# Performance work log

Measured on AMD Instinct MI355X. Metric: run time of the kernel, lower is better.

Reference implementation:

```python
import jax, jax.numpy as jnp
import numpy as np

N_NODES = 50000
N_EDGES = 800000
N_FEATS = 128
E_FEATS = 64
N_OUT = 64
E_OUT = 32
HID = 128  # num_hids = [128]; f lifts node features to this dim
N_STEPS = 3


def _mlp(v, W1, b1, W2, b2):
    # one hidden ReLU layer, linear output (same structure for all 7 transforms)
    return jax.nn.relu(v @ W1 + b1) @ W2 + b2


def _init_mlp(key, d_in, d_hid, d_out, scale=0.05):
    k1, k2 = jax.random.split(key)
    return (jax.random.normal(k1, (d_in, d_hid), jnp.float32) * scale,
            jnp.zeros((d_hid,), jnp.float32),
            jax.random.normal(k2, (d_hid, d_out), jnp.float32) * scale,
            jnp.zeros((d_out,), jnp.float32))


def setup_inputs() -> dict:
    key = jax.random.key(0)
    ks = jax.random.split(key, 10)
    x = jax.random.normal(ks[0], (N_NODES, N_FEATS), jnp.float32)
    xe = jax.random.normal(ks[1], (N_EDGES, E_FEATS), jnp.float32)
    edge_index = jax.random.randint(ks[2], (2, N_EDGES), 0, N_NODES, jnp.int32)
    inp = {"x": x, "xe": xe, "edge_index": edge_index}
    names = ["f", "g", "h", "k1", "k2", "k", "l"]
    dims = {"f": (N_FEATS, HID), "g": (HID, HID), "h": (HID, N_OUT),
            "k1": (HID, HID), "k2": (HID, HID), "k": (E_FEATS, HID), "l": (HID, E_OUT)}
    for i, nm in enumerate(names):
        d_in, d_out = dims[nm]
        W1, b1, W2, b2 = _init_mlp(ks[3 + i], d_in, HID, d_out)
        inp[nm + "_W1"], inp[nm + "_b1"] = W1, b1
        inp[nm + "_W2"], inp[nm + "_b2"] = W2, b2
    return inp


def reference(x, xe, edge_index,
              f_W1, f_b1, f_W2, f_b2,
              g_W1, g_b1, g_W2, g_b2,
              h_W1, h_b1, h_W2, h_b2,
              k1_W1, k1_b1, k1_W2, k1_b2,
              k2_W1, k2_b1, k2_W2, k2_b2,
              k_W1, k_b1, k_W2, k_b2,
              l_W1, l_b1, l_W2, l_b2):
    src, dst = edge_index[0], edge_index[1]
    # 1. y = f(x): lift node features to HID
    y = _mlp(x, f_W1, f_b1, f_W2, f_b2)
    # 2. message passing: y <- g(sum over neighbors of y) + y
    for _ in range(N_STEPS):
        agg = jax.ops.segment_sum(y[src], dst, num_segments=N_NODES)  # [N, HID]
        y = _mlp(agg, g_W1, g_b1, g_W2, g_b2) + y
    # 3. node output z = h(y)
    node_out = _mlp(y, h_W1, h_b1, h_W2, h_b2)  # [N, N_OUT]
    # 4. edge output z_ij = l(k1(y_i) + k2(y_j) + k(x_ij))
    e_hid = (_mlp(y[src], k1_W1, k1_b1, k1_W2, k1_b2)
             + _mlp(y[dst], k2_W1, k2_b1, k2_W2, k2_b2)
             + _mlp(xe, k_W1, k_b1, k_W2, k_b2))  # [E, HID]
    edge_out = _mlp(e_hid, l_W1, l_b1, l_W2, l_b2)  # [E, E_OUT]
    return node_out, edge_out
```

## Files before the change

### kernel.cpp

```cpp
#include <hip/hip_runtime.h>
#include <hip/hip_bf16.h>

namespace {

constexpr int NN = 50000;
constexpr int NE = 800000;

typedef __attribute__((ext_vector_type(8))) short bf16x8;
typedef __attribute__((ext_vector_type(4))) float f32x4;

__device__ __forceinline__ short f2bf(float f) {
  union { __hip_bfloat16 h; short s; } u;
  u.h = __float2bfloat16(f);
  return u.s;
}
__device__ __forceinline__ float bf2f(short s) {
  union { unsigned int u; float f; } v;
  v.u = ((unsigned int)(unsigned short)s) << 16;
  return v.f;
}
__device__ __forceinline__ unsigned int pkbf2(float a, float b) {
  return (unsigned int)(unsigned short)f2bf(a) |
         ((unsigned int)(unsigned short)f2bf(b) << 16);
}

struct WTab {
  const float* W[14];
  short* out[14];
  int din[14];
  int dout[14];
};

__global__ __launch_bounds__(256) void wfrag_all(WTab tab) {
  int wi = blockIdx.y;
  int din = tab.din[wi], dout = tab.dout[wi];
  int total = din * dout;
  int gid = blockIdx.x * 256 + threadIdx.x;
  if (gid >= total) return;
  const float* W = tab.W[wi];
  short* Wf = tab.out[wi];
  int j = gid & 7;
  int l = (gid >> 3) & 63;
  int rest = gid >> 9;
  int nK = din >> 5;
  int kc = rest % nK;
  int t = rest / nK;
  int n = t * 16 + (l & 15);
  int k = kc * 32 + (l >> 4) * 8 + j;
  Wf[gid] = f2bf(W[(size_t)k * dout + n]);
}

__global__ __launch_bounds__(256) void hist_kernel(const int* __restrict__ edst,
                                                   int* __restrict__ deg) {
  int e = blockIdx.x * 256 + threadIdx.x;
  if (e < NE) atomicAdd(&deg[edst[e]], 1);
}

__global__ __launch_bounds__(256) void scan1_kernel(const int* __restrict__ deg,
                                                    int* __restrict__ excl,
                                                    int* __restrict__ bsum, int N) {
  __shared__ int s[256];
  int tid = threadIdx.x;
  int i = blockIdx.x * 256 + tid;
  int v = (i < N) ? deg[i] : 0;
  s[tid] = v;
  __syncthreads();
  for (int d = 1; d < 256; d <<= 1) {
    int t = (tid >= d) ? s[tid - d] : 0;
    __syncthreads();
    s[tid] += t;
    __syncthreads();
  }
  if (i < N) excl[i] = s[tid] - v;
  if (tid == 255) bsum[blockIdx.x] = s[255];
}

__global__ __launch_bounds__(256) void scan2_kernel(const int* __restrict__ bsum,
                                                    int* __restrict__ boff, int nb) {
  __shared__ int s[256];
  int tid = threadIdx.x;
  int v = (tid < nb) ? bsum[tid] : 0;
  s[tid] = v;
  __syncthreads();
  for (int d = 1; d < 256; d <<= 1) {
    int t = (tid >= d) ? s[tid - d] : 0;
    __syncthreads();
    s[tid] += t;
    __syncthreads();
  }
  if (tid <= nb) boff[tid] = s[tid] - v;
}

__global__ __launch_bounds__(256) void scan3_kernel(const int* __restrict__ excl,
                                                    const int* __restrict__ boff,
                                                    int* __restrict__ row_start,
                                                    int N, int nb) {
  int i = blockIdx.x * 256 + threadIdx.x;
  if (i < N) row_start[i] = excl[i] + boff[i >> 8];
  else if (i == N) row_start[N] = boff[nb];
}

__global__ __launch_bounds__(256) void fill_kernel(const int* __restrict__ esrc,
                                                   const int* __restrict__ edst,
                                                   const int* __restrict__ row_start,
                                                   int* __restrict__ cursor,
                                                   int* __restrict__ adj) {
  int e = blockIdx.x * 256 + threadIdx.x;
  if (e >= NE) return;
  int d = edst[e];
  int p = atomicAdd(&cursor[d], 1);
  adj[row_start[d] + p] = esrc[e];
}

__global__ __launch_bounds__(256) void agg_kernel(const ushort* __restrict__ yb,
                                                  const int* __restrict__ row_start,
                                                  const int* __restrict__ adj,
                                                  ushort* __restrict__ aggb) {
  int gid = blockIdx.x * 256 + threadIdx.x;
  int lane = gid & 63;
  int g = lane >> 4;
  int q = lane & 15;
  int n = (gid >> 6) * 4 + g;
  int s0 = row_start[n], s1 = row_start[n + 1];
  float a0 = 0, a1 = 0, a2 = 0, a3 = 0, a4 = 0, a5 = 0, a6 = 0, a7 = 0;
  for (int base = s0; base < s1; base += 16) {
    int idx = 0;
    if (base + q < s1) idx = adj[base + q];
    int cnt = s1 - base;
    if (cnt > 16) cnt = 16;
#pragma unroll
    for (int j = 0; j < 16; ++j) {
      if (j < cnt) {
        int s = __shfl(idx, g * 16 + j);
        uint4 v = *reinterpret_cast<const uint4*>(yb + (size_t)s * 128 + q * 8);
        a0 += bf2f((short)(v.x & 0xffff)); a1 += bf2f((short)(v.x >> 16));
        a2 += bf2f((short)(v.y & 0xffff)); a3 += bf2f((short)(v.y >> 16));
        a4 += bf2f((short)(v.z & 0xffff)); a5 += bf2f((short)(v.z >> 16));
        a6 += bf2f((short)(v.w & 0xffff)); a7 += bf2f((short)(v.w >> 16));
      }
    }
  }
  uint4 o;
  o.x = pkbf2(a0, a1);
  o.y = pkbf2(a2, a3);
  o.z = pkbf2(a4, a5);
  o.w = pkbf2(a6, a7);
  *reinterpret_cast<uint4*>(aggb + (size_t)n * 128 + q * 8) = o;
}


template <int NG, int NTHR>
__device__ __forceinline__ void wcopy(short* dst, const short* __restrict__ src,
                                      int tid) {
#pragma unroll
  for (int g0 = 0; g0 < NG; g0 += NTHR) {
    int g = g0 + tid;
    if (g < NG)
      *reinterpret_cast<bf16x8*>(dst + (size_t)g * 8) =
          *reinterpret_cast<const bf16x8*>(src + (size_t)g * 8);
  }
}

template <int KCPH, int NT>
__device__ __forceinline__ void gemm16(const char* tb, const short* wbuf,
                                       int rbase, int lane, f32x4 (&acc)[NT]) {
#pragma unroll
  for (int kc = 0; kc < KCPH; ++kc) {
    int row = rbase + (lane & 15);
    int off = (row * 256 + kc * 64 + (lane >> 4) * 16) ^ ((row & 7) << 4);
    bf16x8 a = *reinterpret_cast<const bf16x8*>(tb + off);
#pragma unroll
    for (int t = 0; t < NT; ++t) {
      bf16x8 b = *reinterpret_cast<const bf16x8*>(wbuf + ((size_t)((t * KCPH + kc) * 64 + lane)) * 8);
      acc[t] = __builtin_amdgcn_mfma_f32_16x16x32_bf16(a, b, acc[t], 0, 0, 0);
    }
  }
}

template <int NT>
__device__ __forceinline__ void zero16(f32x4 (&acc)[NT]) {
  const f32x4 vzero = {0.f, 0.f, 0.f, 0.f};
#pragma unroll
  for (int t = 0; t < NT; ++t) acc[t] = vzero;
}

template <int NT, bool RELU>
__device__ __forceinline__ void epi16(char* dst, int rbase, int lane,
                                      const float* bias, f32x4 (&acc)[NT]) {
#pragma unroll
  for (int t = 0; t < NT; ++t) {
    int col = t * 16 + (lane & 15);
    float bb = bias[col];
#pragma unroll
    for (int i = 0; i < 4; ++i) {
      int row = rbase + (lane >> 4) * 4 + i;
      float h = acc[t][i] + bb;
      if (RELU) h = fmaxf(h, 0.f);
      int off = (row * 256 + col * 2) ^ ((row & 7) << 4);
      *reinterpret_cast<short*>(dst + off) = f2bf(h);
    }
  }
}

template <bool INBF16, bool SKIP, bool WY, int NOUT, bool OUTF32>
__global__ __launch_bounds__(1024, 1) void mlp_big(
    const void* __restrict__ Xv,
    const short* __restrict__ W1f, const float* __restrict__ b1,
    const short* __restrict__ W2f, const float* __restrict__ b2,
    float* __restrict__ y, ushort* __restrict__ bfout,
    float* __restrict__ fout, int nrows) {
  __shared__ alignas(16) short tile_[256 * 128];
  __shared__ alignas(16) short wb1[16384];
  constexpr int NG2 = (NOUT == 128) ? 2048 : 1024;
  __shared__ alignas(16) short wb2[NG2 * 8];
  char* tb = reinterpret_cast<char*>(tile_);
  const int tid = threadIdx.x;
  const int lane = tid & 63;
  const int wave = tid >> 6;
  const int row0 = blockIdx.x * 256;
  const int wbase = wave * 16;

  wcopy<2048, 1024>(wb1, W1f, tid);
  wcopy<NG2, 1024>(wb2, W2f, tid);
  __syncthreads();

  if constexpr (INBF16) {
    const ushort* X = (const ushort*)Xv;
#pragma unroll
    for (int it = 0; it < 4; ++it) {
      int idx = it * 64 + lane;
      int r = wbase + (idx >> 4);
      int c = idx & 15;
      int gr = row0 + r;
      bf16x8 v = {};
      if (gr < nrows) v = *reinterpret_cast<const bf16x8*>(X + (size_t)gr * 128 + c * 8);
      int off = (r * 256 + c * 16) ^ ((r & 7) << 4);
      *reinterpret_cast<bf16x8*>(tb + off) = v;
    }
  } else {
    const float* X = (const float*)Xv;
#pragma unroll
    for (int it = 0; it < 8; ++it) {
      int idx = it * 64 + lane;
      int r = wbase + (idx >> 5);
      int c = idx & 31;
      int gr = row0 + r;
      float4 v = make_float4(0.f, 0.f, 0.f, 0.f);
      if (gr < nrows) v = *reinterpret_cast<const float4*>(X + (size_t)gr * 128 + c * 4);
      short4 p;
      p.x = f2bf(v.x); p.y = f2bf(v.y); p.z = f2bf(v.z); p.w = f2bf(v.w);
      int off = (r * 256 + c * 8) ^ ((r & 7) << 4);
      *reinterpret_cast<short4*>(tb + off) = p;
    }
  }

  f32x4 acc[8];
  zero16(acc);
  gemm16<4, 8>(tb, wb1, wbase, lane, acc);
  epi16<8, true>(tb, wbase, lane, b1, acc);

  constexpr int NT2 = NOUT / 16;
  f32x4 acc2[NT2];
  zero16(acc2);
  gemm16<4, NT2>(tb, wb2, wbase, lane, acc2);

  if constexpr (OUTF32) {
#pragma unroll
    for (int t = 0; t < NT2; ++t) {
      int col = t * 16 + (lane & 15);
      float bb = b2[col];
#pragma unroll
      for (int i = 0; i < 4; ++i) {
        int row = wbase + (lane >> 4) * 4 + i;
        int gr = row0 + row;
        if (gr < nrows) fout[(size_t)gr * NOUT + col] = acc2[t][i] + bb;
      }
    }
  } else {
#pragma unroll
    for (int t = 0; t < NT2; ++t) {
      int col = t * 16 + (lane & 15);
      float bb = b2[col];
#pragma unroll
      for (int i = 0; i < 4; ++i) {
        int row = wbase + (lane >> 4) * 4 + i;
        int gr = row0 + row;
        if (gr < nrows) {
          float v = acc2[t][i] + bb;
          if constexpr (SKIP) v += y[(size_t)gr * 128 + col];
          if constexpr (WY) y[(size_t)gr * 128 + col] = v;
          int off = (row * 256 + col * 2) ^ ((row & 7) << 4);
          *reinterpret_cast<short*>(tb + off) = f2bf(v);
        }
      }
    }
#pragma unroll
    for (int rr = 0; rr < 16; ++rr) {
      int row = wbase + rr;
      int gr = row0 + row;
      if (gr < nrows) {
        int off = (row * 256 + lane * 4) ^ ((row & 7) << 4);
        unsigned int v = *reinterpret_cast<const unsigned int*>(tb + off);
        *reinterpret_cast<unsigned int*>(bfout + (size_t)gr * 128 + lane * 2) = v;
      }
    }
  }
}

__device__ __forceinline__ void load_tile_regs(const float* __restrict__ xe,
                                               const int* __restrict__ esrc,
                                               const int* __restrict__ edst,
                                               int ebase, int lane,
                                               int& vint, float4 (&xr)[4]) {
  vint = (lane < 32) ? esrc[ebase + (lane & 15)] : edst[ebase + (lane & 15)];
#pragma unroll
  for (int i = 0; i < 4; ++i) {
    int idx = i * 64 + lane;
    int r = idx >> 4, c = idx & 15;
    xr[i] = *reinterpret_cast<const float4*>(xe + (size_t)(ebase + r) * 64 + c * 4);
  }
}

__global__ __launch_bounds__(1024, 1) void edge_kernel(
    const float* __restrict__ xe, const int* __restrict__ esrc,
    const int* __restrict__ edst, const ushort* __restrict__ u1b,
    const ushort* __restrict__ u2b,
    const short* __restrict__ kW1f, const float* __restrict__ kb1,
    const short* __restrict__ kW2f, const float* __restrict__ kb2,
    const short* __restrict__ lW1f, const float* __restrict__ lb1,
    const short* __restrict__ lW2f, const float* __restrict__ lb2,
    float* __restrict__ out) {
  __shared__ alignas(16) short wK1[8192];
  __shared__ alignas(16) short wK2[16384];
  __shared__ alignas(16) short wL1[16384];
  __shared__ alignas(16) short wL2[4096];
  __shared__ alignas(16) short tile_[256 * 128];
  __shared__ float biasL[416];
  char* tb = reinterpret_cast<char*>(tile_);
  const int tid = threadIdx.x;
  const int lane = tid & 63;
  const int wave = tid >> 6;
  const int f4 = lane & 31;
  const int hs = lane >> 5;
  const int wbase = wave * 16;

  wcopy<1024, 1024>(wK1, kW1f, tid);
  wcopy<2048, 1024>(wK2, kW2f, tid);
  wcopy<2048, 1024>(wL1, lW1f, tid);
  wcopy<512, 1024>(wL2, lW2f, tid);
  if (tid < 128) biasL[tid] = kb1[tid];
  else if (tid < 256) biasL[tid] = kb2[tid - 128];
  else if (tid < 384) biasL[tid] = lb1[tid - 256];
  else if (tid < 416) biasL[tid] = lb2[tid - 384];
  __syncthreads();

  constexpr int NTILES = NE / 256;
  int tile = blockIdx.x;
  int vnext;
  float4 xr[4];
  load_tile_regs(xe, esrc, edst, tile * 256 + wbase, lane, vnext, xr);

  for (; tile < NTILES; tile += gridDim.x) {
    const int ebase = tile * 256 + wbase;
    const int vcur = vnext;

#pragma unroll
    for (int i = 0; i < 4; ++i) {
      int idx = i * 64 + lane;
      int r = wbase + (idx >> 4), c = idx & 15;
      short4 p;
      p.x = f2bf(xr[i].x); p.y = f2bf(xr[i].y);
      p.z = f2bf(xr[i].z); p.w = f2bf(xr[i].w);
      int off = (r * 256 + c * 8) ^ ((r & 7) << 4);
      *reinterpret_cast<short4*>(tb + off) = p;
    }

    ushort4 ga[4], gb[4];
#pragma unroll
    for (int i = 0; i < 4; ++i) {
      int s = __shfl(vcur, i * 2 + hs);
      int d = __shfl(vcur, 32 + i * 2 + hs);
      ga[i] = *reinterpret_cast<const ushort4*>(u1b + (size_t)s * 128 + f4 * 4);
      gb[i] = *reinterpret_cast<const ushort4*>(u2b + (size_t)d * 128 + f4 * 4);
    }

    f32x4 acc[8];
    zero16(acc);
    gemm16<2, 8>(tb, wK1, wbase, lane, acc);
    epi16<8, true>(tb, wbase, lane, &biasL[0], acc);

    ushort4 ga2[4], gb2[4];
#pragma unroll
    for (int i = 0; i < 4; ++i) {
      int s = __shfl(vcur, (4 + i) * 2 + hs);
      int d = __shfl(vcur, 32 + (4 + i) * 2 + hs);
      ga2[i] = *reinterpret_cast<const ushort4*>(u1b + (size_t)s * 128 + f4 * 4);
      gb2[i] = *reinterpret_cast<const ushort4*>(u2b + (size_t)d * 128 + f4 * 4);
    }
    uint2 gsum[8];
#pragma unroll
    for (int i = 0; i < 4; ++i) {
      float s0 = bf2f((short)ga[i].x) + bf2f((short)gb[i].x);
      float s1 = bf2f((short)ga[i].y) + bf2f((short)gb[i].y);
      float s2 = bf2f((short)ga[i].z) + bf2f((short)gb[i].z);
      float s3 = bf2f((short)ga[i].w) + bf2f((short)gb[i].w);
      gsum[i] = make_uint2(pkbf2(s0, s1), pkbf2(s2, s3));
    }

    zero16(acc);
    gemm16<4, 8>(tb, wK2, wbase, lane, acc);
    epi16<8, false>(tb, wbase, lane, &biasL[128], acc);

#pragma unroll
    for (int i = 0; i < 4; ++i) {
      float s0 = bf2f((short)ga2[i].x) + bf2f((short)gb2[i].x);
      float s1 = bf2f((short)ga2[i].y) + bf2f((short)gb2[i].y);
      float s2 = bf2f((short)ga2[i].z) + bf2f((short)gb2[i].z);
      float s3 = bf2f((short)ga2[i].w) + bf2f((short)gb2[i].w);
      gsum[4 + i] = make_uint2(pkbf2(s0, s1), pkbf2(s2, s3));
    }

#pragma unroll
    for (int i = 0; i < 8; ++i) {
      int r = wbase + i * 2 + hs;
      int off = (r * 256 + f4 * 8) ^ ((r & 7) << 4);
      short4 c = *reinterpret_cast<short4*>(tb + off);
      uint2 g = gsum[i];
      short4 nw;
      nw.x = f2bf(bf2f(c.x) + bf2f((short)(g.x & 0xffff)));
      nw.y = f2bf(bf2f(c.y) + bf2f((short)(g.x >> 16)));
      nw.z = f2bf(bf2f(c.z) + bf2f((short)(g.y & 0xffff)));
      nw.w = f2bf(bf2f(c.w) + bf2f((short)(g.y >> 16)));
      *reinterpret_cast<short4*>(tb + off) = nw;
    }

    int nt2 = tile + gridDim.x;
    if (nt2 < NTILES)
      load_tile_regs(xe, esrc, edst, nt2 * 256 + wbase, lane, vnext, xr);

    zero16(acc);
    gemm16<4, 8>(tb, wL1, wbase, lane, acc);
    epi16<8, true>(tb, wbase, lane, &biasL[256], acc);

    f32x4 acc4[2];
    zero16(acc4);
    gemm16<4, 2>(tb, wL2, wbase, lane, acc4);

#pragma unroll
    for (int t = 0; t < 2; ++t) {
      int col = t * 16 + (lane & 15);
      float bb = biasL[384 + col];
#pragma unroll
      for (int i = 0; i < 4; ++i) {
        int row = (lane >> 4) * 4 + i;
        out[(size_t)(ebase + row) * 32 + col] = acc4[t][i] + bb;
      }
    }
  }
}

}

extern "C" void kernel_launch(void* const* d_in, const int* in_sizes, int n_in,
                              void* d_out, int out_size, void* d_ws, size_t ws_size,
                              hipStream_t stream) {
  const float* x = (const float*)d_in[0];
  const float* xe = (const float*)d_in[1];
  const int* eidx = (const int*)d_in[2];
  const int* esrc = eidx;
  const int* edst = eidx + NE;

  const float* fb1 = (const float*)d_in[4];
  const float* fb2 = (const float*)d_in[6];
  const float* gb1 = (const float*)d_in[8];
  const float* gb2 = (const float*)d_in[10];
  const float* hb1 = (const float*)d_in[12];
  const float* hb2 = (const float*)d_in[14];
  const float* k1b1 = (const float*)d_in[16];
  const float* k1b2 = (const float*)d_in[18];
  const float* k2b1 = (const float*)d_in[20];
  const float* k2b2 = (const float*)d_in[22];
  const float* kb1 = (const float*)d_in[24];
  const float* kb2 = (const float*)d_in[26];
  const float* lb1 = (const float*)d_in[28];
  const float* lb2 = (const float*)d_in[30];

  char* ws = (char*)d_ws;
  size_t off = 0;
  auto alloc = [&](size_t bytes) -> void* {
    void* p = ws + off;
    off = (off + bytes + 255) & ~(size_t)255;
    return p;
  };
  float* y = (float*)alloc((size_t)NN * 128 * 4);
  ushort* ybA = (ushort*)alloc((size_t)NN * 128 * 2);
  ushort* ybB = (ushort*)alloc((size_t)NN * 128 * 2);
  ushort* aggb = (ushort*)alloc((size_t)NN * 128 * 2);
  ushort* u1b = (ushort*)alloc((size_t)NN * 128 * 2);
  ushort* u2b = (ushort*)alloc((size_t)NN * 128 * 2);
  int* deg = (int*)alloc((size_t)NN * 4);
  int* excl = (int*)alloc((size_t)NN * 4);
  int* bsum = (int*)alloc(256 * 4);
  int* boff = (int*)alloc(256 * 4);
  int* row_start = (int*)alloc((size_t)(NN + 16) * 4);
  int* cursor = (int*)alloc((size_t)NN * 4);
  int* adj = (int*)alloc((size_t)NE * 4);

  const int wi[14] = {3, 5, 7, 9, 11, 13, 15, 17, 19, 21, 23, 25, 27, 29};
  const int wdin[14] = {128, 128, 128, 128, 128, 128, 128, 128, 128, 128, 64, 128, 128, 128};
  const int wdout[14] = {128, 128, 128, 128, 128, 64, 128, 128, 128, 128, 128, 128, 128, 32};
  WTab tab;
  short* wf[14];
  for (int i = 0; i < 14; ++i) {
    size_t elems = (size_t)wdin[i] * wdout[i];
    wf[i] = (short*)alloc(elems * 2);
    tab.W[i] = (const float*)d_in[wi[i]];
    tab.out[i] = wf[i];
    tab.din[i] = wdin[i];
    tab.dout[i] = wdout[i];
  }
  wfrag_all<<<dim3(64, 14, 1), 256, 0, stream>>>(tab);

  short* fW1f = wf[0];  short* fW2f = wf[1];
  short* gW1f = wf[2];  short* gW2f = wf[3];
  short* hW1f = wf[4];  short* hW2f = wf[5];
  short* k1W1f = wf[6]; short* k1W2f = wf[7];
  short* k2W1f = wf[8]; short* k2W2f = wf[9];
  short* kW1f = wf[10]; short* kW2f = wf[11];
  short* lW1f = wf[12]; short* lW2f = wf[13];

  const int nb = (NN + 255) / 256;
  hipMemsetAsync(deg, 0, (size_t)NN * 4, stream);
  hist_kernel<<<(NE + 255) / 256, 256, 0, stream>>>(edst, deg);
  scan1_kernel<<<nb, 256, 0, stream>>>(deg, excl, bsum, NN);
  scan2_kernel<<<1, 256, 0, stream>>>(bsum, boff, nb);
  scan3_kernel<<<(NN + 256) / 256 + 1, 256, 0, stream>>>(excl, boff, row_start, NN, nb);
  hipMemsetAsync(cursor, 0, (size_t)NN * 4, stream);
  fill_kernel<<<(NE + 255) / 256, 256, 0, stream>>>(esrc, edst, row_start, cursor, adj);

  const int nblk = (NN + 255) / 256;

  mlp_big<false, false, true, 128, false><<<nblk, 1024, 0, stream>>>(
      x, fW1f, fb1, fW2f, fb2, y, ybA, nullptr, NN);

  ushort* ybin = ybA;
  ushort* ybout = ybB;
  for (int s = 0; s < 3; ++s) {
    agg_kernel<<<(NN / 4 * 64) / 256, 256, 0, stream>>>(ybin, row_start, adj, aggb);
    mlp_big<true, true, true, 128, false><<<nblk, 1024, 0, stream>>>(
        aggb, gW1f, gb1, gW2f, gb2, y, ybout, nullptr, NN);
    ushort* t = ybin; ybin = ybout; ybout = t;
  }

  mlp_big<true, false, false, 128, false><<<nblk, 1024, 0, stream>>>(
      ybin, k1W1f, k1b1, k1W2f, k1b2, nullptr, u1b, nullptr, NN);
  mlp_big<true, false, false, 128, false><<<nblk, 1024, 0, stream>>>(
      ybin, k2W1f, k2b1, k2W2f, k2b2, nullptr, u2b, nullptr, NN);

  mlp_big<true, false, false, 64, true><<<nblk, 1024, 0, stream>>>(
      ybin, hW1f, hb1, hW2f, hb2, nullptr, nullptr, (float*)d_out, NN);

  float* edge_out = (float*)d_out + (size_t)NN * 64;
  edge_kernel<<<256, 1024, 0, stream>>>(xe, esrc, edst, u1b, u2b, kW1f, kb1, kW2f, kb2,
                                        lW1f, lb1, lW2f, lb2, edge_out);
}
```

Before: 482.5 us.

## Merge tail MLPs into one grid launch, add MFMA priority, drop edge prefetch

The three tail node MLPs (k1, k2, h) now run as one launch with blockIdx.y choosing which weights to use, replacing three separate launches. This removes launch gaps and lets the three small grids fill the GPU together. The GEMM inner loop raises wave priority around the MFMA burst with s_setprio. The edge kernel also drops its register prefetch of the next tile's xe and indices and loads them inline instead, which may expose memory latency but frees registers.

```diff
diff --git a/kernel.cpp b/kernel.cpp
--- a/kernel.cpp
+++ b/kernel.cpp
@@ -169,11 +169,13 @@
     int row = rbase + (lane & 15);
     int off = (row * 256 + kc * 64 + (lane >> 4) * 16) ^ ((row & 7) << 4);
     bf16x8 a = *reinterpret_cast<const bf16x8*>(tb + off);
+    __builtin_amdgcn_s_setprio(1);
 #pragma unroll
     for (int t = 0; t < NT; ++t) {
       bf16x8 b = *reinterpret_cast<const bf16x8*>(wbuf + ((size_t)((t * KCPH + kc) * 64 + lane)) * 8);
       acc[t] = __builtin_amdgcn_mfma_f32_16x16x32_bf16(a, b, acc[t], 0, 0, 0);
     }
+    __builtin_amdgcn_s_setprio(0);
   }
 }
 
@@ -202,17 +204,15 @@
   }
 }
 
-template <bool INBF16, bool SKIP, bool WY, int NOUT, bool OUTF32>
+template <bool INBF16, bool SKIP, bool WY>
 __global__ __launch_bounds__(1024, 1) void mlp_big(
     const void* __restrict__ Xv,
     const short* __restrict__ W1f, const float* __restrict__ b1,
     const short* __restrict__ W2f, const float* __restrict__ b2,
-    float* __restrict__ y, ushort* __restrict__ bfout,
-    float* __restrict__ fout, int nrows) {
+    float* __restrict__ y, ushort* __restrict__ bfout, int nrows) {
   __shared__ alignas(16) short tile_[256 * 128];
   __shared__ alignas(16) short wb1[16384];
-  constexpr int NG2 = (NOUT == 128) ? 2048 : 1024;
-  __shared__ alignas(16) short wb2[NG2 * 8];
+  __shared__ alignas(16) short wb2[16384];
   char* tb = reinterpret_cast<char*>(tile_);
   const int tid = threadIdx.x;
   const int lane = tid & 63;
@@ -221,7 +221,7 @@
   const int wbase = wave * 16;
 
   wcopy<2048, 1024>(wb1, W1f, tid);
-  wcopy<NG2, 1024>(wb2, W2f, tid);
+  wcopy<2048, 1024>(wb2, W2f, tid);
   __syncthreads();
 
   if constexpr (INBF16) {
@@ -259,41 +259,93 @@
   gemm16<4, 8>(tb, wb1, wbase, lane, acc);
   epi16<8, true>(tb, wbase, lane, b1, acc);
 
-  constexpr int NT2 = NOUT / 16;
-  f32x4 acc2[NT2];
+  f32x4 acc2[8];
   zero16(acc2);
-  gemm16<4, NT2>(tb, wb2, wbase, lane, acc2);
-
-  if constexpr (OUTF32) {
-#pragma unroll
-    for (int t = 0; t < NT2; ++t) {
-      int col = t * 16 + (lane & 15);
-      float bb = b2[col];
-#pragma unroll
-      for (int i = 0; i < 4; ++i) {
-        int row = wbase + (lane >> 4) * 4 + i;
-        int gr = row0 + row;
-        if (gr < nrows) fout[(size_t)gr * NOUT + col] = acc2[t][i] + bb;
+  gemm16<4, 8>(tb, wb2, wbase, lane, acc2);
+
+#pragma unroll
+  for (int t = 0; t < 8; ++t) {
+    int col = t * 16 + (lane & 15);
+    float bb = b2[col];
+#pragma unroll
+    for (int i = 0; i < 4; ++i) {
+      int row = wbase + (lane >> 4) * 4 + i;
+      int gr = row0 + row;
+      if (gr < nrows) {
+        float v = acc2[t][i] + bb;
+        if constexpr (SKIP) v += y[(size_t)gr * 128 + col];
+        if constexpr (WY) y[(size_t)gr * 128 + col] = v;
+        int off = (row * 256 + col * 2) ^ ((row & 7) << 4);
+        *reinterpret_cast<short*>(tb + off) = f2bf(v);
       }
     }
-  } else {
-#pragma unroll
-    for (int t = 0; t < NT2; ++t) {
-      int col = t * 16 + (lane & 15);
-      float bb = b2[col];
-#pragma unroll
-      for (int i = 0; i < 4; ++i) {
-        int row = wbase + (lane >> 4) * 4 + i;
-        int gr = row0 + row;
-        if (gr < nrows) {
-          float v = acc2[t][i] + bb;
-          if constexpr (SKIP) v += y[(size_t)gr * 128 + col];
-          if constexpr (WY) y[(size_t)gr * 128 + col] = v;
-          int off = (row * 256 + col * 2) ^ ((row & 7) << 4);
-          *reinterpret_cast<short*>(tb + off) = f2bf(v);
-        }
-      }
-    }
+  }
+#pragma unroll
+  for (int rr = 0; rr < 16; ++rr) {
+    int row = wbase + rr;
+    int gr = row0 + row;
+    if (gr < nrows) {
+      int off = (row * 256 + lane * 4) ^ ((row & 7) << 4);
+      unsigned int v = *reinterpret_cast<const unsigned int*>(tb + off);
+      *reinterpret_cast<unsigned int*>(bfout + (size_t)gr * 128 + lane * 2) = v;
+    }
+  }
+}
+
+__global__ __launch_bounds__(1024, 1) void mlp_tail3(
+    const ushort* __restrict__ X,
+    const short* __restrict__ k1W1f, const float* __restrict__ k1b1,
+    const short* __restrict__ k1W2f, const float* __restrict__ k1b2,
+    const short* __restrict__ k2W1f, const float* __restrict__ k2b1,
+    const short* __restrict__ k2W2f, const float* __restrict__ k2b2,
+    const short* __restrict__ hW1f, const float* __restrict__ hb1,
+    const short* __restrict__ hW2f, const float* __restrict__ hb2,
+    ushort* __restrict__ u1b, ushort* __restrict__ u2b,
+    float* __restrict__ node_out, int nrows) {
+  __shared__ alignas(16) short tile_[256 * 128];
+  __shared__ alignas(16) short wb1[16384];
+  __shared__ alignas(16) short wb2[16384];
+  char* tb = reinterpret_cast<char*>(tile_);
+  const int tid = threadIdx.x;
+  const int lane = tid & 63;
+  const int wave = tid >> 6;
+  const int row0 = blockIdx.x * 256;
+  const int wbase = wave * 16;
+  const int mode = blockIdx.y;
+
+  const short* W1f = (mode == 0) ? k1W1f : (mode == 1) ? k2W1f : hW1f;
+  const float* b1 = (mode == 0) ? k1b1 : (mode == 1) ? k2b1 : hb1;
+  const short* W2f = (mode == 0) ? k1W2f : (mode == 1) ? k2W2f : hW2f;
+  const float* b2 = (mode == 0) ? k1b2 : (mode == 1) ? k2b2 : hb2;
+
+  wcopy<2048, 1024>(wb1, W1f, tid);
+  if (mode < 2) wcopy<2048, 1024>(wb2, W2f, tid);
+  else wcopy<1024, 1024>(wb2, W2f, tid);
+  __syncthreads();
+
+#pragma unroll
+  for (int it = 0; it < 4; ++it) {
+    int idx = it * 64 + lane;
+    int r = wbase + (idx >> 4);
+    int c = idx & 15;
+    int gr = row0 + r;
+    bf16x8 v = {};
+    if (gr < nrows) v = *reinterpret_cast<const bf16x8*>(X + (size_t)gr * 128 + c * 8);
+    int off = (r * 256 + c * 16) ^ ((r & 7) << 4);
+    *reinterpret_cast<bf16x8*>(tb + off) = v;
+  }
+
+  f32x4 acc[8];
+  zero16(acc);
+  gemm16<4, 8>(tb, wb1, wbase, lane, acc);
+  epi16<8, true>(tb, wbase, lane, b1, acc);
+
+  if (mode < 2) {
+    f32x4 acc2[8];
+    zero16(acc2);
+    gemm16<4, 8>(tb, wb2, wbase, lane, acc2);
+    epi16<8, false>(tb, wbase, lane, b2, acc2);
+    ushort* ub = (mode == 0) ? u1b : u2b;
 #pragma unroll
     for (int rr = 0; rr < 16; ++rr) {
       int row = wbase + rr;
@@ -301,23 +353,24 @@
       if (gr < nrows) {
         int off = (row * 256 + lane * 4) ^ ((row & 7) << 4);
         unsigned int v = *reinterpret_cast<const unsigned int*>(tb + off);
-        *reinterpret_cast<unsigned int*>(bfout + (size_t)gr * 128 + lane * 2) = v;
+        *reinterpret_cast<unsigned int*>(ub + (size_t)gr * 128 + lane * 2) = v;
       }
     }
-  }
-}
-
-__device__ __forceinline__ void load_tile_regs(const float* __restrict__ xe,
-                                               const int* __restrict__ esrc,
-                                               const int* __restrict__ edst,
-                                               int ebase, int lane,
-                                               int& vint, float4 (&xr)[4]) {
-  vint = (lane < 32) ? esrc[ebase + (lane & 15)] : edst[ebase + (lane & 15)];
-#pragma unroll
-  for (int i = 0; i < 4; ++i) {
-    int idx = i * 64 + lane;
-    int r = idx >> 4, c = idx & 15;
-    xr[i] = *reinterpret_cast<const float4*>(xe + (size_t)(ebase + r) * 64 + c * 4);
+  } else {
+    f32x4 acc2[4];
+    zero16(acc2);
+    gemm16<4, 4>(tb, wb2, wbase, lane, acc2);
+#pragma unroll
+    for (int t = 0; t < 4; ++t) {
+      int col = t * 16 + (lane & 15);
+      float bb = b2[col];
+#pragma unroll
+      for (int i = 0; i < 4; ++i) {
+        int row = wbase + (lane >> 4) * 4 + i;
+        int gr = row0 + row;
+        if (gr < nrows) node_out[(size_t)gr * 64 + col] = acc2[t][i] + bb;
+      }
+    }
   }
 }
 
@@ -355,23 +408,22 @@
   __syncthreads();
 
   constexpr int NTILES = NE / 256;
-  int tile = blockIdx.x;
-  int vnext;
-  float4 xr[4];
-  load_tile_regs(xe, esrc, edst, tile * 256 + wbase, lane, vnext, xr);
-
-  for (; tile < NTILES; tile += gridDim.x) {
+
+  for (int tile = blockIdx.x; tile < NTILES; tile += gridDim.x) {
     const int ebase = tile * 256 + wbase;
-    const int vcur = vnext;
+
+    const int vcur = (lane < 32) ? esrc[ebase + (lane & 15)] : edst[ebase + (lane & 15)];
 
 #pragma unroll
     for (int i = 0; i < 4; ++i) {
       int idx = i * 64 + lane;
-      int r = wbase + (idx >> 4), c = idx & 15;
+      int r = idx >> 4, c = idx & 15;
+      float4 v = *reinterpret_cast<const float4*>(xe + (size_t)(ebase + r) * 64 + c * 4);
       short4 p;
-      p.x = f2bf(xr[i].x); p.y = f2bf(xr[i].y);
-      p.z = f2bf(xr[i].z); p.w = f2bf(xr[i].w);
-      int off = (r * 256 + c * 8) ^ ((r & 7) << 4);
+      p.x = f2bf(v.x); p.y = f2bf(v.y);
+      p.z = f2bf(v.z); p.w = f2bf(v.w);
+      int rr = wbase + r;
+      int off = (rr * 256 + c * 8) ^ ((rr & 7) << 4);
       *reinterpret_cast<short4*>(tb + off) = p;
     }
 
@@ -433,10 +485,6 @@
       nw.w = f2bf(bf2f(c.w) + bf2f((short)(g.y >> 16)));
       *reinterpret_cast<short4*>(tb + off) = nw;
     }
-
-    int nt2 = tile + gridDim.x;
-    if (nt2 < NTILES)
-      load_tile_regs(xe, esrc, edst, nt2 * 256 + wbase, lane, vnext, xr);
 
     zero16(acc);
     gemm16<4, 8>(tb, wL1, wbase, lane, acc);
@@ -540,25 +588,21 @@
 
   const int nblk = (NN + 255) / 256;
 
-  mlp_big<false, false, true, 128, false><<<nblk, 1024, 0, stream>>>(
-      x, fW1f, fb1, fW2f, fb2, y, ybA, nullptr, NN);
+  mlp_big<false, false, true><<<nblk, 1024, 0, stream>>>(
+      x, fW1f, fb1, fW2f, fb2, y, ybA, NN);
 
   ushort* ybin = ybA;
   ushort* ybout = ybB;
   for (int s = 0; s < 3; ++s) {
     agg_kernel<<<(NN / 4 * 64) / 256, 256, 0, stream>>>(ybin, row_start, adj, aggb);
-    mlp_big<true, true, true, 128, false><<<nblk, 1024, 0, stream>>>(
-        aggb, gW1f, gb1, gW2f, gb2, y, ybout, nullptr, NN);
+    mlp_big<true, true, true><<<nblk, 1024, 0, stream>>>(
+        aggb, gW1f, gb1, gW2f, gb2, y, ybout, NN);
     ushort* t = ybin; ybin = ybout; ybout = t;
   }
 
-  mlp_big<true, false, false, 128, false><<<nblk, 1024, 0, stream>>>(
-      ybin, k1W1f, k1b1, k1W2f, k1b2, nullptr, u1b, nullptr, NN);
-  mlp_big<true, false, false, 128, false><<<nblk, 1024, 0, stream>>>(
-      ybin, k2W1f, k2b1, k2W2f, k2b2, nullptr, u2b, nullptr, NN);
-
-  mlp_big<true, false, false, 64, true><<<nblk, 1024, 0, stream>>>(
-      ybin, hW1f, hb1, hW2f, hb2, nullptr, nullptr, (float*)d_out, NN);
+  mlp_tail3<<<dim3(nblk, 3), 1024, 0, stream>>>(
+      ybin, k1W1f, k1b1, k1W2f, k1b2, k2W1f, k2b1, k2W2f, k2b2,
+      hW1f, hb1, hW2f, hb2, u1b, u2b, (float*)d_out, NN);
 
   float* edge_out = (float*)d_out + (size_t)NN * 64;
   edge_kernel<<<256, 1024, 0, stream>>>(xe, esrc, edst, u1b, u2b, kW1f, kb1, kW2f, kb2,
```

Result: slower. 504.6 us (+4.6%).
